# Kernel tuning notes

Measured on AMD Instinct MI355X. Metric: run time of the kernel, lower is better.

The kernel has to match this reference:

```python
import jax, jax.numpy as jnp
import numpy as np

# ---- Cl(3,0,1) algebra tables (metric: e0^2=0, e1^2=e2^2=e3^2=1) ----
def _cayley(metric):
    n = len(metric); dim = 1 << n
    C = np.zeros((dim, dim, dim), np.float32)
    for a in range(dim):
        for b in range(dim):
            s = 1.0
            for i in range(n):
                if (b >> i) & 1:
                    # sign from moving e_i past higher-index generators of a
                    s *= (-1.0) ** bin(a >> (i + 1)).count('1')
                    if (a >> i) & 1:
                        s *= metric[i]  # contraction e_i e_i = metric[i]
            C[a, b, a ^ b] = s
    return C

_METRIC_CPU = [0.0, 1.0, 1.0, 1.0]  # Cl(3,0,1)
CAYLEY = jnp.asarray(_cayley(_METRIC_CPU))  # [16,16,16]
_grades = np.array([bin(i).count('1') for i in range(16)])
GRADE_MASK = jnp.asarray((_grades[None, :] == np.arange(5)[:, None]).astype(np.float32))  # [5,16]

B, N, D, K, M = 8, 65536, 16, 8, 8
CTRL_DIM, HID = 4, 64
EPS = 1e-12

def setup_inputs() -> dict:
    key = jax.random.key(0)
    ks = jax.random.split(key, 12)
    in_dim = 5 + CTRL_DIM  # num_grades + ctrl dim
    return {
        'cpu_state': jax.random.normal(ks[0], (B, N, D), jnp.float32),
        'ctrl_cursor': jax.random.normal(ks[1], (B, CTRL_DIM), jnp.float32),
        'rule_memory': jax.random.normal(ks[2], (B, M, D), jnp.float32),
        'templates': jax.random.normal(ks[3], (K, D), jnp.float32) * 0.01,
        'W1': jax.random.normal(ks[4], (in_dim, HID), jnp.float32) / np.sqrt(in_dim),
        'b1': jnp.zeros((HID,), jnp.float32),
        'W2': jax.random.normal(ks[5], (HID, K), jnp.float32) / np.sqrt(HID),
        'b2': jnp.zeros((K,), jnp.float32),
        'Wr': jax.random.normal(ks[6], (D, K * D), jnp.float32) / np.sqrt(D),
        'br': jnp.zeros((K * D,), jnp.float32),
        'log_temperature': jnp.zeros((), jnp.float32),  # log(1.0)
    }

def reference(cpu_state, ctrl_cursor, rule_memory, templates, W1, b1, W2, b2, Wr, br, log_temperature):
    # summary + per-grade norms of the mean multivector
    cpu_summary = cpu_state.mean(axis=1)                                  # [B,16]
    grade_norms = jnp.sqrt(jnp.einsum('gd,bd->bg', GRADE_MASK, cpu_summary**2) + EPS)  # [B,5]
    score_input = jnp.concatenate([grade_norms, ctrl_cursor], axis=-1)    # [B,9]
    scores = jax.nn.relu(score_input @ W1 + b1) @ W2 + b2                 # [B,K]

    # rule modulation of templates
    rule_summary = rule_memory.mean(axis=1)                               # [B,16]
    rule_mod = (rule_summary @ Wr + br).reshape(rule_summary.shape[0], K, D)
    templ = templates[None, :, :] + rule_mod                              # [B,K,16]
    instructions = scores[..., None] * templ                              # [B,K,16]

    # execute_all: geometric product of each instruction with every cpu cell
    # (a*b)_l = a_i b_j CAYLEY[i,j,l]; small [B,K,16,16] operator then apply to state
    op = jnp.einsum('bki,ijl->bkjl', instructions, CAYLEY)                # [B,K,16,16]
    outcomes = jnp.einsum('bkjl,bnj->bknl', op, cpu_state)                # [B,K,N,16]

    # gumbel-softmax soft routing
    tau = jnp.clip(jnp.exp(log_temperature), 0.1, 5.0)
    u = jax.random.uniform(jax.random.key(42), scores.shape, jnp.float32, 1e-6, 1.0 - 1e-6)
    g = -jnp.log(-jnp.log(u))
    weights = jax.nn.softmax((scores + g) / tau, axis=-1)                 # [B,K]

    new_cpu_state = jnp.einsum('bk,bknd->bnd', weights, outcomes)         # [B,N,16]
    return new_cpu_state
```

## Files before the change

### kernel.cpp

```cpp
#include <hip/hip_runtime.h>


#define B_ 8
#define N_ 65536
#define D_ 16
#define K_ 8
#define M_ 8
#define HID_ 64
#define BLK_PER_B 64
#define ROWS_PER_BLK (N_ / BLK_PER_B)

struct SgnTab { float v[16][16]; };
constexpr SgnTab make_sgn() {
  SgnTab t{};
  for (int a = 0; a < 16; a++)
    for (int b = 0; b < 16; b++) {
      float s = 1.0f;
      for (int i = 0; i < 4; i++)
        if ((b >> i) & 1) {
          int h = a >> (i + 1), pc = 0;
          for (int q = 0; q < 4; q++) pc += (h >> q) & 1;
          if (pc & 1) s = -s;
          if ((a >> i) & 1) s *= (i == 0 ? 0.0f : 1.0f);
        }
      t.v[a][b] = s;
    }
  return t;
}
constexpr SgnTab SGN = make_sgn();

__device__ __forceinline__ unsigned rotl32(unsigned x, int n) {
  return (x << n) | (x >> (32 - n));
}
__device__ void threefry2x32(unsigned k0, unsigned k1, unsigned& x0, unsigned& x1) {
  unsigned ks0 = k0, ks1 = k1, ks2 = k0 ^ k1 ^ 0x1BD11BDAu;
  x0 += ks0; x1 += ks1;
  const int rotA[4] = {13, 15, 26, 6};
  const int rotB[4] = {17, 29, 16, 24};
#define TF_R4(rot)                                      \
  _Pragma("unroll")                                     \
  for (int r = 0; r < 4; r++) {                         \
    x0 += x1; x1 = rotl32(x1, rot[r]); x1 ^= x0;        \
  }
  TF_R4(rotA); x0 += ks1; x1 += ks2 + 1u;
  TF_R4(rotB); x0 += ks2; x1 += ks0 + 2u;
  TF_R4(rotA); x0 += ks0; x1 += ks1 + 3u;
  TF_R4(rotB); x0 += ks1; x1 += ks2 + 4u;
  TF_R4(rotA); x0 += ks2; x1 += ks0 + 5u;
#undef TF_R4
}

__global__ __launch_bounds__(256) void k1_reduce(
    const float* __restrict__ cpu, float* __restrict__ partial) {
  const int b = blockIdx.y, blk = blockIdx.x, t = threadIdx.x;
  const float4* base =
      (const float4*)(cpu + (((size_t)b << 16) + (size_t)blk * ROWS_PER_BLK) * D_);
  float a0 = 0.f, a1 = 0.f, a2 = 0.f, a3 = 0.f;
#pragma unroll
  for (int i = 0; i < (ROWS_PER_BLK * 4) / 256; i++) {
    float4 v = base[i * 256 + t];
    a0 += v.x; a1 += v.y; a2 += v.z; a3 += v.w;
  }
  __shared__ float red[256 * 4];
  red[t * 4 + 0] = a0; red[t * 4 + 1] = a1;
  red[t * 4 + 2] = a2; red[t * 4 + 3] = a3;
  __syncthreads();
  if (t < 16) {
    const int c = t >> 2, j = t & 3;
    float s = 0.f;
#pragma unroll
    for (int m = 0; m < 64; m++) s += red[(c + 4 * m) * 4 + j];
    partial[((size_t)b * BLK_PER_B + blk) * 16 + t] = s;
  }
}

__global__ __launch_bounds__(256) void k2_small(
    const float* __restrict__ partial,
    const float* __restrict__ ctrl,
    const float* __restrict__ rulemem,
    const float* __restrict__ templates,
    const float* __restrict__ W1,
    const float* __restrict__ b1,
    const float* __restrict__ W2,
    const float* __restrict__ b2,
    const float* __restrict__ Wr,
    const float* __restrict__ br,
    const float* __restrict__ logt,
    float* __restrict__ comb) {
  const int t = threadIdx.x;
  __shared__ float summary[8][16], rs[8][16], gn[8][5], h[8][64], sc[8][8];
  __shared__ float instr[8][8][16], g64[64], wts[8][8];
  __shared__ float redA[8][16][16];

  {
    float acc[8];
#pragma unroll
    for (int b = 0; b < 8; b++) acc[b] = 0.f;
#pragma unroll
    for (int c = 0; c < 32; c++)
      acc[c >> 2] += partial[c * 256 + t];
#pragma unroll
    for (int b = 0; b < 8; b++) redA[b][t >> 4][t & 15] = acc[b];
  }
  __syncthreads();
  if (t < 128) {
    const int b = t >> 4, d = t & 15;
    float s = 0.f;
#pragma unroll
    for (int g = 0; g < 16; g++) s += redA[b][g][d];
    summary[b][d] = s * (1.0f / (float)N_);
    float rsum = 0.f;
    for (int m = 0; m < M_; m++) rsum += rulemem[(b * M_ + m) * 16 + d];
    rs[b][d] = rsum * (1.0f / (float)M_);
  }
  __syncthreads();
  if (t < 40) {
    const int b = t / 5, g = t % 5;
    float s = 0.f;
    for (int d = 0; d < 16; d++)
      if (__popc(d) == g) { float v = summary[b][d]; s += v * v; }
    gn[b][g] = sqrtf(s + 1e-12f);
  }
  __syncthreads();
  for (int idx = t; idx < B_ * HID_; idx += 256) {
    const int b = idx >> 6, j = idx & 63;
    float a = b1[j];
    for (int i = 0; i < 9; i++) {
      float in = (i < 5) ? gn[b][i] : ctrl[b * 4 + (i - 5)];
      a += in * W1[i * HID_ + j];
    }
    h[b][j] = fmaxf(a, 0.f);
  }
  __syncthreads();
  if (t < 64) {
    const int b = t >> 3, k = t & 7;
    float a = b2[k];
    for (int j = 0; j < HID_; j++) a += h[b][j] * W2[j * K_ + k];
    sc[b][k] = a;
  }
  __syncthreads();
  for (int idx = t; idx < B_ * K_ * 16; idx += 256) {
    const int b = idx >> 7, k = (idx >> 4) & 7, d = idx & 15;
    float a = br[k * 16 + d];
    for (int j = 0; j < 16; j++) a += rs[b][j] * Wr[j * 128 + k * 16 + d];
    instr[b][k][d] = sc[b][k] * (templates[k * 16 + d] + a);
  }
  if (t < 64) {
    unsigned x0 = 0u, x1 = (unsigned)t;
    threefry2x32(0u, 42u, x0, x1);
    unsigned bits = x0 ^ x1;
    float f01 = __uint_as_float((bits >> 9) | 0x3f800000u) - 1.0f;
    float u = fmaxf(1e-6f, f01 * (1.0f - 2e-6f) + 1e-6f);
    g64[t] = -logf(-logf(u));
  }
  __syncthreads();
  if (t < 8) {
    float lt = logt[0];
    float tau = fminf(fmaxf(expf(lt), 0.1f), 5.0f);
    float z[8], m = -1e30f;
    for (int k = 0; k < 8; k++) {
      z[k] = (sc[t][k] + g64[t * 8 + k]) / tau;
      m = fmaxf(m, z[k]);
    }
    float ssum = 0.f;
    for (int k = 0; k < 8; k++) { z[k] = expf(z[k] - m); ssum += z[k]; }
    for (int k = 0; k < 8; k++) wts[t][k] = z[k] / ssum;
  }
  __syncthreads();
  if (t < 128) {
    const int b = t >> 4, i = t & 15;
    float s = 0.f;
    for (int k = 0; k < 8; k++) s += wts[b][k] * instr[b][k][i];
    comb[b * 16 + i] = s;
  }
}

__global__ __launch_bounds__(256) void k3_apply(
    const float* __restrict__ cpu, const float* __restrict__ comb,
    float* __restrict__ out) {
  const int b = blockIdx.x >> 8;
  const int rowInB = ((blockIdx.x & 255) << 8) + threadIdx.x;
  const size_t row = ((size_t)b << 16) + (size_t)rowInB;

  float cb[16];
  const float* cp = comb + b * 16;
#pragma unroll
  for (int i = 0; i < 16; i++) cb[i] = cp[i];

  const float4* p = (const float4*)(cpu + row * D_);
  float4 v0 = p[0], v1 = p[1], v2 = p[2], v3 = p[3];
  float x[16] = {v0.x, v0.y, v0.z, v0.w, v1.x, v1.y, v1.z, v1.w,
                 v2.x, v2.y, v2.z, v2.w, v3.x, v3.y, v3.z, v3.w};

  float o[16];
#pragma unroll
  for (int l = 0; l < 16; l++) {
    float acc = 0.f;
#pragma unroll
    for (int j = 0; j < 16; j++) {
      const float s = SGN.v[j ^ l][j];
      if (s > 0.5f)       acc = fmaf(cb[j ^ l], x[j], acc);
      else if (s < -0.5f) acc = fmaf(-cb[j ^ l], x[j], acc);
    }
    o[l] = acc;
  }

  float4* q = (float4*)(out + row * D_);
  q[0] = make_float4(o[0],  o[1],  o[2],  o[3]);
  q[1] = make_float4(o[4],  o[5],  o[6],  o[7]);
  q[2] = make_float4(o[8],  o[9],  o[10], o[11]);
  q[3] = make_float4(o[12], o[13], o[14], o[15]);
}

extern "C" void kernel_launch(void* const* d_in, const int* in_sizes, int n_in,
                              void* d_out, int out_size, void* d_ws, size_t ws_size,
                              hipStream_t stream) {
  const float* cpu       = (const float*)d_in[0];
  const float* ctrl      = (const float*)d_in[1];
  const float* rulemem   = (const float*)d_in[2];
  const float* templates = (const float*)d_in[3];
  const float* W1        = (const float*)d_in[4];
  const float* b1        = (const float*)d_in[5];
  const float* W2        = (const float*)d_in[6];
  const float* b2        = (const float*)d_in[7];
  const float* Wr        = (const float*)d_in[8];
  const float* br        = (const float*)d_in[9];
  const float* logt      = (const float*)d_in[10];

  float* partial = (float*)d_ws;
  float* comb    = partial + (size_t)B_ * BLK_PER_B * 16;

  k1_reduce<<<dim3(BLK_PER_B, B_), 256, 0, stream>>>(cpu, partial);
  k2_small<<<1, 256, 0, stream>>>(partial, ctrl, rulemem, templates, W1, b1,
                                  W2, b2, Wr, br, logt, comb);
  k3_apply<<<2048, 256, 0, stream>>>(cpu, comb, (float*)d_out);
}
```

Measured before the change: 117.6 us.

## Fuse small scoring kernel into apply kernel, recomputing per-block combined operator

Removes the single-block k2_small launch. Each of the 2048 apply blocks now loads the weights into shared memory and redundantly recomputes the batch's summary, MLP scores, Gumbel weights and combined instruction before applying it to its rows. This drops one launch and its serial dependency gap, at the cost of redundant per-block work, extra global reads of the weights, several barriers before the main load, and heavier shared-memory use that may lower occupancy.

```diff
diff --git a/kernel.cpp b/kernel.cpp
--- a/kernel.cpp
+++ b/kernel.cpp
@@ -74,7 +74,8 @@
   }
 }
 
-__global__ __launch_bounds__(256) void k2_small(
+__global__ __launch_bounds__(256) void k3_comb_apply(
+    const float* __restrict__ cpu,
     const float* __restrict__ partial,
     const float* __restrict__ ctrl,
     const float* __restrict__ rulemem,
@@ -86,106 +87,111 @@
     const float* __restrict__ Wr,
     const float* __restrict__ br,
     const float* __restrict__ logt,
-    float* __restrict__ comb) {
+    float* __restrict__ out) {
   const int t = threadIdx.x;
-  __shared__ float summary[8][16], rs[8][16], gn[8][5], h[8][64], sc[8][8];
-  __shared__ float instr[8][8][16], g64[64], wts[8][8];
-  __shared__ float redA[8][16][16];
+  const int b = blockIdx.x >> 8;
+  const int rowInB = ((blockIdx.x & 255) << 8) + t;
+  const size_t row = ((size_t)b << 16) + (size_t)rowInB;
+
+  __shared__ float sW1[9 * 64], sb1[64], sW2[64 * 8], sb2[8];
+  __shared__ float sWr[16 * 128], sbr[128], stpl[128];
+  __shared__ float srm_b[128], sctrl_b[4], slogt;
+  __shared__ float red2[256 * 4];
+  __shared__ float summary[16], rs[16], gn[5], h[HID_], sc[8];
+  __shared__ float instr[8][16], g8[8], wts[8], comb_s[16];
 
   {
-    float acc[8];
-#pragma unroll
-    for (int b = 0; b < 8; b++) acc[b] = 0.f;
-#pragma unroll
-    for (int c = 0; c < 32; c++)
-      acc[c >> 2] += partial[c * 256 + t];
-#pragma unroll
-    for (int b = 0; b < 8; b++) redA[b][t >> 4][t & 15] = acc[b];
-  }
-  __syncthreads();
-  if (t < 128) {
-    const int b = t >> 4, d = t & 15;
-    float s = 0.f;
-#pragma unroll
-    for (int g = 0; g < 16; g++) s += redA[b][g][d];
-    summary[b][d] = s * (1.0f / (float)N_);
+    float4 pp = ((const float4*)(partial + (size_t)b * 1024))[t];
+    for (int i = t; i < 9 * 64; i += 256) sW1[i] = W1[i];
+    for (int i = t; i < 64 * 8; i += 256) sW2[i] = W2[i];
+    for (int i = t; i < 16 * 128; i += 256) sWr[i] = Wr[i];
+    if (t < 64) sb1[t] = b1[t];
+    if (t < 8) sb2[t] = b2[t];
+    if (t < 128) sbr[t] = br[t];
+    if (t < 128) stpl[t] = templates[t];
+    if (t < 128) srm_b[t] = rulemem[b * 128 + t];
+    if (t < 4) sctrl_b[t] = ctrl[b * 4 + t];
+    if (t == 0) slogt = logt[0];
+    red2[t * 4 + 0] = pp.x; red2[t * 4 + 1] = pp.y;
+    red2[t * 4 + 2] = pp.z; red2[t * 4 + 3] = pp.w;
+  }
+  __syncthreads();
+  if (t < 16) {
+    const int c = t >> 2, j = t & 3;
+    float s = 0.f;
+#pragma unroll
+    for (int m = 0; m < 64; m++) s += red2[(c + 4 * m) * 4 + j];
+    summary[t] = s * (1.0f / (float)N_);
     float rsum = 0.f;
-    for (int m = 0; m < M_; m++) rsum += rulemem[(b * M_ + m) * 16 + d];
-    rs[b][d] = rsum * (1.0f / (float)M_);
-  }
-  __syncthreads();
-  if (t < 40) {
-    const int b = t / 5, g = t % 5;
-    float s = 0.f;
+#pragma unroll
+    for (int m = 0; m < M_; m++) rsum += srm_b[m * 16 + t];
+    rs[t] = rsum * (1.0f / (float)M_);
+  }
+  __syncthreads();
+  if (t < 5) {
+    float s = 0.f;
+#pragma unroll
     for (int d = 0; d < 16; d++)
-      if (__popc(d) == g) { float v = summary[b][d]; s += v * v; }
-    gn[b][g] = sqrtf(s + 1e-12f);
-  }
-  __syncthreads();
-  for (int idx = t; idx < B_ * HID_; idx += 256) {
-    const int b = idx >> 6, j = idx & 63;
-    float a = b1[j];
+      if (__popc(d) == t) { float v = summary[d]; s += v * v; }
+    gn[t] = sqrtf(s + 1e-12f);
+  }
+  __syncthreads();
+  if (t < HID_) {
+    float a = sb1[t];
+#pragma unroll
     for (int i = 0; i < 9; i++) {
-      float in = (i < 5) ? gn[b][i] : ctrl[b * 4 + (i - 5)];
-      a += in * W1[i * HID_ + j];
-    }
-    h[b][j] = fmaxf(a, 0.f);
-  }
-  __syncthreads();
-  if (t < 64) {
-    const int b = t >> 3, k = t & 7;
-    float a = b2[k];
-    for (int j = 0; j < HID_; j++) a += h[b][j] * W2[j * K_ + k];
-    sc[b][k] = a;
-  }
-  __syncthreads();
-  for (int idx = t; idx < B_ * K_ * 16; idx += 256) {
-    const int b = idx >> 7, k = (idx >> 4) & 7, d = idx & 15;
-    float a = br[k * 16 + d];
-    for (int j = 0; j < 16; j++) a += rs[b][j] * Wr[j * 128 + k * 16 + d];
-    instr[b][k][d] = sc[b][k] * (templates[k * 16 + d] + a);
-  }
-  if (t < 64) {
-    unsigned x0 = 0u, x1 = (unsigned)t;
+      float in = (i < 5) ? gn[i] : sctrl_b[i - 5];
+      a += in * sW1[i * HID_ + t];
+    }
+    h[t] = fmaxf(a, 0.f);
+  }
+  __syncthreads();
+  if (t < 8) {
+    float a = sb2[t];
+#pragma unroll
+    for (int j = 0; j < HID_; j++) a += h[j] * sW2[j * K_ + t];
+    sc[t] = a;
+    unsigned x0 = 0u, x1 = (unsigned)(b * 8 + t);
     threefry2x32(0u, 42u, x0, x1);
     unsigned bits = x0 ^ x1;
     float f01 = __uint_as_float((bits >> 9) | 0x3f800000u) - 1.0f;
     float u = fmaxf(1e-6f, f01 * (1.0f - 2e-6f) + 1e-6f);
-    g64[t] = -logf(-logf(u));
-  }
-  __syncthreads();
-  if (t < 8) {
-    float lt = logt[0];
-    float tau = fminf(fmaxf(expf(lt), 0.1f), 5.0f);
+    g8[t] = -logf(-logf(u));
+  }
+  __syncthreads();
+  if (t < 128) {
+    const int k = t >> 4, d = t & 15;
+    float a = sbr[k * 16 + d];
+#pragma unroll
+    for (int j = 0; j < 16; j++) a += rs[j] * sWr[j * 128 + k * 16 + d];
+    instr[k][d] = sc[k] * (stpl[k * 16 + d] + a);
+  }
+  if (t == 0) {
+    float tau = fminf(fmaxf(expf(slogt), 0.1f), 5.0f);
     float z[8], m = -1e30f;
+#pragma unroll
     for (int k = 0; k < 8; k++) {
-      z[k] = (sc[t][k] + g64[t * 8 + k]) / tau;
+      z[k] = (sc[k] + g8[k]) / tau;
       m = fmaxf(m, z[k]);
     }
     float ssum = 0.f;
+#pragma unroll
     for (int k = 0; k < 8; k++) { z[k] = expf(z[k] - m); ssum += z[k]; }
-    for (int k = 0; k < 8; k++) wts[t][k] = z[k] / ssum;
-  }
-  __syncthreads();
-  if (t < 128) {
-    const int b = t >> 4, i = t & 15;
-    float s = 0.f;
-    for (int k = 0; k < 8; k++) s += wts[b][k] * instr[b][k][i];
-    comb[b * 16 + i] = s;
-  }
-}
-
-__global__ __launch_bounds__(256) void k3_apply(
-    const float* __restrict__ cpu, const float* __restrict__ comb,
-    float* __restrict__ out) {
-  const int b = blockIdx.x >> 8;
-  const int rowInB = ((blockIdx.x & 255) << 8) + threadIdx.x;
-  const size_t row = ((size_t)b << 16) + (size_t)rowInB;
+#pragma unroll
+    for (int k = 0; k < 8; k++) wts[k] = z[k] / ssum;
+  }
+  __syncthreads();
+  if (t < 16) {
+    float s = 0.f;
+#pragma unroll
+    for (int k = 0; k < 8; k++) s += wts[k] * instr[k][t];
+    comb_s[t] = s;
+  }
+  __syncthreads();
 
   float cb[16];
-  const float* cp = comb + b * 16;
-#pragma unroll
-  for (int i = 0; i < 16; i++) cb[i] = cp[i];
+#pragma unroll
+  for (int i = 0; i < 16; i++) cb[i] = comb_s[i];
 
   const float4* p = (const float4*)(cpu + row * D_);
   float4 v0 = p[0], v1 = p[1], v2 = p[2], v3 = p[3];
@@ -228,10 +234,9 @@
   const float* logt      = (const float*)d_in[10];
 
   float* partial = (float*)d_ws;
-  float* comb    = partial + (size_t)B_ * BLK_PER_B * 16;
 
   k1_reduce<<<dim3(BLK_PER_B, B_), 256, 0, stream>>>(cpu, partial);
-  k2_small<<<1, 256, 0, stream>>>(partial, ctrl, rulemem, templates, W1, b1,
-                                  W2, b2, Wr, br, logt, comb);
-  k3_apply<<<2048, 256, 0, stream>>>(cpu, comb, (float*)d_out);
-}
+  k3_comb_apply<<<2048, 256, 0, stream>>>(cpu, partial, ctrl, rulemem,
+                                          templates, W1, b1, W2, b2, Wr, br,
+                                          logt, (float*)d_out);
+}
```

After: 122.8 us. 4.4% more time.
